# Kernel optimization log

Hardware: AMD Instinct MI355X
Metric: run time of the kernel (lower is better)

The kernel has to match this reference:

```python
import jax, jax.numpy as jnp
import numpy as np

B = 8192
DB, DA, DE, DM, DS = 512, 256, 256, 512, 512
IN = DB + DA + DE + DM + DS  # 2048
F = 2048


def _ternary_linear(x, w, b):
    # BitNet-b1.58 absmean quantization with straight-through estimator.
    s = jnp.mean(jnp.abs(w))
    wq = jnp.round(jnp.clip(w / (s + 1e-5), -1.0, 1.0)) * s
    wq = w + jax.lax.stop_gradient(wq - w)  # STE
    return x @ wq.T + b


def _layernorm(x, g, b, eps=1e-5):
    m = jnp.mean(x, axis=-1, keepdims=True)
    v = jnp.mean((x - m) ** 2, axis=-1, keepdims=True)
    return (x - m) * jax.lax.rsqrt(v + eps) * g + b


def _gelu(x):
    return jax.nn.gelu(x, approximate=False)  # torch nn.GELU default (erf)


def setup_inputs() -> dict:
    key = jax.random.key(0)
    ks = jax.random.split(key, 16)
    w = lambda k, o, i: (jax.random.normal(k, (o, i), dtype=jnp.float32) * 0.02)
    return {
        "z_byte": jax.random.normal(ks[0], (B, DB), dtype=jnp.float32),
        "z_addr": jax.random.normal(ks[1], (B, DA), dtype=jnp.float32),
        "z_evt": jax.random.normal(ks[2], (B, DE), dtype=jnp.float32),
        "z_map": jax.random.normal(ks[3], (B, DM), dtype=jnp.float32),
        "z_sum": jax.random.normal(ks[4], (B, DS), dtype=jnp.float32),
        "gate_w1": w(ks[5], F, IN), "gate_b1": jnp.zeros((F,), jnp.float32),
        "gate_w2": w(ks[6], F, F), "gate_b2": jnp.zeros((F,), jnp.float32),
        "tr_w1": w(ks[7], F, IN), "tr_b1": jnp.zeros((F,), jnp.float32),
        "tr_w2": w(ks[8], F, F), "tr_b2": jnp.zeros((F,), jnp.float32),
        "mlp_w1": w(ks[9], 2 * F, F), "mlp_b1": jnp.zeros((2 * F,), jnp.float32),
        "mlp_w2": w(ks[10], F, 2 * F), "mlp_b2": jnp.zeros((F,), jnp.float32),
        "ln1_g": jnp.ones((F,), jnp.float32), "ln1_b": jnp.zeros((F,), jnp.float32),
        "ln2_g": jnp.ones((F,), jnp.float32), "ln2_b": jnp.zeros((F,), jnp.float32),
    }


def reference(z_byte, z_addr, z_evt, z_map, z_sum,
              gate_w1, gate_b1, gate_w2, gate_b2,
              tr_w1, tr_b1, tr_w2, tr_b2,
              mlp_w1, mlp_b1, mlp_w2, mlp_b2,
              ln1_g, ln1_b, ln2_g, ln2_b):
    combined = jnp.concatenate([z_byte, z_addr, z_evt, z_map, z_sum], axis=-1)  # [B, IN]
    g = _ternary_linear(_gelu(_ternary_linear(combined, gate_w1, gate_b1)), gate_w2, gate_b2)
    t = _ternary_linear(_gelu(_ternary_linear(combined, tr_w1, tr_b1)), tr_w2, tr_b2)
    fused = jax.nn.sigmoid(g * 1.2) * t
    fused = _layernorm(fused, ln1_g, ln1_b)
    mlp = _gelu(fused @ mlp_w1.T + mlp_b1) @ mlp_w2.T + mlp_b2
    return _layernorm(fused + mlp, ln2_g, ln2_b)
```

## Files before the change

### kernel.cpp

```cpp
#include <hip/hip_runtime.h>

typedef unsigned short u16;
typedef unsigned int u32;
typedef __bf16 bf16x8 __attribute__((ext_vector_type(8)));
typedef float f32x4 __attribute__((ext_vector_type(4)));
typedef const __attribute__((address_space(3))) u16* ldsp;

#define B_ROWS 8192

__device__ __forceinline__ float bf2f(u16 h) {
    union { u32 u; float f; } v; v.u = ((u32)h) << 16; return v.f;
}
__device__ __forceinline__ u16 f2bf(float f) {
    union { float f; u32 u; } v; v.f = f;
    u32 r = v.u + 0x7fffu + ((v.u >> 16) & 1u);
    return (u16)(r >> 16);
}
__device__ __forceinline__ float gelu_fast(float x) {
    float u = x * (0.7978845608f + 0.0356774081f * x * x);
    float e = __expf(2.f * u);
    float th = 1.f - 2.f / (e + 1.f);
    return 0.5f * x * (1.f + th);
}
__device__ __forceinline__ float sigmoid12(float g) {
    return 1.f / (1.f + __expf(-1.2f * g));
}
__device__ __forceinline__ float wave_reduce_sum(float v) {
    #pragma unroll
    for (int m = 32; m; m >>= 1) v += __shfl_xor(v, m, 64);
    return v;
}
__device__ __forceinline__ void async16(const void* g, void* l) {
    __builtin_amdgcn_global_load_lds((const __attribute__((address_space(1))) u32*)g,
                                     (__attribute__((address_space(3))) u32*)l, 16, 0, 0);
}
template<int OFF>
__device__ __forceinline__ bf16x8 dsr(ldsp a) {
    bf16x8 r;
    asm volatile("ds_read_b128 %0, %1 offset:%c2"
                 : "=v"(r) : "v"(a), "i"(OFF) : "memory");
    return r;
}

__global__ void absmean1_kernel(const float* __restrict__ w0, const float* __restrict__ w1,
                                const float* __restrict__ w2, const float* __restrict__ w3,
                                float* __restrict__ partials) {
    const float* w = (blockIdx.y == 0) ? w0 : (blockIdx.y == 1) ? w1 : (blockIdx.y == 2) ? w2 : w3;
    int base = blockIdx.x * 16384;
    float acc = 0.f;
    for (int j = threadIdx.x; j < 16384; j += 256) {
        float4 v = ((const float4*)w)[base + j];
        acc += fabsf(v.x) + fabsf(v.y) + fabsf(v.z) + fabsf(v.w);
    }
    acc = wave_reduce_sum(acc);
    __shared__ float red[4];
    int lane = threadIdx.x & 63, wv = threadIdx.x >> 6;
    if (lane == 0) red[wv] = acc;
    __syncthreads();
    if (threadIdx.x == 0)
        partials[blockIdx.y * 64 + blockIdx.x] = red[0] + red[1] + red[2] + red[3];
}

__global__ void absmean2_kernel(const float* __restrict__ partials, double* __restrict__ sums) {
    float v = partials[blockIdx.x * 64 + threadIdx.x];
    v = wave_reduce_sum(v);
    if (threadIdx.x == 0) sums[blockIdx.x] = (double)v;
}

__global__ void prep_kernel(const float* __restrict__ w0, const float* __restrict__ w1,
                            const float* __restrict__ w2, const float* __restrict__ w3,
                            const float* __restrict__ mw1, const float* __restrict__ mw2,
                            u16* __restrict__ wq, u16* __restrict__ mwq,
                            const double* __restrict__ sums) {
    int y = blockIdx.y;
    int i = blockIdx.x * 256 + threadIdx.x;
    if (y < 4) {
        const float* w = (y == 0) ? w0 : (y == 1) ? w1 : (y == 2) ? w2 : w3;
        float s = (float)(sums[y] * (1.0 / 4194304.0));
        float den = s + 1e-5f;
        float4 v = ((const float4*)w)[i];
        ushort4 o;
        o.x = f2bf(rintf(fminf(fmaxf(v.x / den, -1.f), 1.f)));
        o.y = f2bf(rintf(fminf(fmaxf(v.y / den, -1.f), 1.f)));
        o.z = f2bf(rintf(fminf(fmaxf(v.z / den, -1.f), 1.f)));
        o.w = f2bf(rintf(fminf(fmaxf(v.w / den, -1.f), 1.f)));
        ((ushort4*)(wq + (size_t)y * 4194304))[i] = o;
    } else {
        const float* src = (y == 4) ? mw1 : mw2;
        u16* dst = mwq + (y == 4 ? 0 : 8388608);
        #pragma unroll
        for (int r = 0; r < 2; ++r) {
            int j = i + r * 1048576;
            float4 v = ((const float4*)src)[j];
            ushort4 o = {f2bf(v.x), f2bf(v.y), f2bf(v.z), f2bf(v.w)};
            ((ushort4*)dst)[j] = o;
        }
    }
}

__global__ void concat_kernel(const float* __restrict__ zb, const float* __restrict__ za,
                              const float* __restrict__ ze, const float* __restrict__ zm,
                              const float* __restrict__ zs, u16* __restrict__ out) {
    int row = blockIdx.x, t = threadIdx.x;
    int col = t * 8;
    const float* src; int scol, stride;
    if (col < 512)       { src = zb; scol = col;        stride = 512; }
    else if (col < 768)  { src = za; scol = col - 512;  stride = 256; }
    else if (col < 1024) { src = ze; scol = col - 768;  stride = 256; }
    else if (col < 1536) { src = zm; scol = col - 1024; stride = 512; }
    else                 { src = zs; scol = col - 1536; stride = 512; }
    const float4* s4 = (const float4*)(src + (size_t)row * stride + scol);
    float4 a = s4[0], b = s4[1];
    ushort4 p0 = {f2bf(a.x), f2bf(a.y), f2bf(a.z), f2bf(a.w)};
    ushort4 p1 = {f2bf(b.x), f2bf(b.y), f2bf(b.z), f2bf(b.w)};
    u16* o = out + (size_t)row * 2048 + col;
    *(ushort4*)o = p0;
    *(ushort4*)(o + 4) = p1;
}

#define STG_A(d, h, kt_) { \
    async16(Ab0 + (size_t)(h) * ha + (size_t)(kt_) * 64, &lds[0][d][h][ci0 * 8]); \
    async16(Ab1 + (size_t)(h) * ha + (size_t)(kt_) * 64, &lds[0][d][h][ci1 * 8]); }
#define STG_B(d, h, kt_) { \
    async16(Wb0 + (size_t)(h) * hw + (size_t)(kt_) * 64, &lds[1][d][h][ci0 * 8]); \
    async16(Wb1 + (size_t)(h) * hw + (size_t)(kt_) * 64, &lds[1][d][h][ci1 * 8]); }
#define AOFF(d, qm, fm) (((d) * 2 + (qm)) * 16384 + (fm) * 2048)
#define BOFF(d, qn, fn) (((d) * 2 + (qn)) * 16384 + (fn) * 2048)
#define LDA_ALL(d, qm) { \
    af[0][0] = dsr<AOFF(d,qm,0)>(vA0); af[0][1] = dsr<AOFF(d,qm,0)>(vA1); \
    af[1][0] = dsr<AOFF(d,qm,1)>(vA0); af[1][1] = dsr<AOFF(d,qm,1)>(vA1); \
    af[2][0] = dsr<AOFF(d,qm,2)>(vA0); af[2][1] = dsr<AOFF(d,qm,2)>(vA1); \
    af[3][0] = dsr<AOFF(d,qm,3)>(vA0); af[3][1] = dsr<AOFF(d,qm,3)>(vA1); }
#define LDB_H(d, qn) { \
    bf[qn][0][0] = dsr<BOFF(d,qn,0)>(vB0); bf[qn][0][1] = dsr<BOFF(d,qn,0)>(vB1); \
    bf[qn][1][0] = dsr<BOFF(d,qn,1)>(vB0); bf[qn][1][1] = dsr<BOFF(d,qn,1)>(vB1); }
#define MFMA_PH(qm, qn) { \
    _Pragma("unroll") for (int fm = 0; fm < 4; ++fm) \
    _Pragma("unroll") for (int fn = 0; fn < 2; ++fn) { \
        acc[qm][qn][fm][fn] = __builtin_amdgcn_mfma_f32_16x16x32_bf16(af[fm][0], bf[qn][fn][0], acc[qm][qn][fm][fn], 0, 0, 0); \
        acc[qm][qn][fm][fn] = __builtin_amdgcn_mfma_f32_16x16x32_bf16(af[fm][1], bf[qn][fn][1], acc[qm][qn][fm][fn], 0, 0, 0); } }
#define PH_TAIL(qm, qn) \
    __builtin_amdgcn_s_barrier(); \
    asm volatile("s_waitcnt lgkmcnt(0)" ::: "memory"); \
    __builtin_amdgcn_sched_barrier(0); \
    __builtin_amdgcn_s_setprio(1); \
    MFMA_PH(qm, qn); \
    __builtin_amdgcn_s_setprio(0); \
    __builtin_amdgcn_s_barrier();
#define GROUP(ktv, d, e) { \
    LDA_ALL(d, 0); LDB_H(d, 0); \
    if ((ktv) + 1 < NT) { STG_B(e, 0, (ktv) + 1); STG_A(e, 1, (ktv) + 1); } \
    PH_TAIL(0, 0); \
    LDB_H(d, 1); \
    PH_TAIL(0, 1); \
    LDA_ALL(d, 1); \
    if ((ktv) + 2 < NT) STG_A(d, 0, (ktv) + 2); \
    PH_TAIL(1, 1); \
    if ((ktv) + 2 < NT) STG_B(d, 1, (ktv) + 2); \
    __builtin_amdgcn_s_barrier(); \
    __builtin_amdgcn_s_setprio(1); \
    MFMA_PH(1, 0); \
    __builtin_amdgcn_s_setprio(0); \
    if ((ktv) < NT - 2)       { asm volatile("s_waitcnt vmcnt(4)" ::: "memory"); } \
    else if ((ktv) == NT - 2) { asm volatile("s_waitcnt vmcnt(0)" ::: "memory"); } \
    __builtin_amdgcn_s_barrier(); }

template<int EPI>
__global__ __launch_bounds__(512, 2) void gemm256(
        const u16* __restrict__ A, const u16* __restrict__ A2, int lda,
        const u16* __restrict__ W, int wz,
        const float* __restrict__ bias0, const float* __restrict__ bias1,
        void* out, void* out2,
        const double* sum0, const double* sum1,
        int N, int K, int ncut) {
    __shared__ __align__(16) u16 lds[2][2][2][8192];
    if (blockIdx.z) { A = A2; W += wz; out = out2; bias0 = bias1; sum0 = sum1; }

    const int t = threadIdx.x;
    const int l = t & 63;
    const int w = t >> 6;
    const int lr = l & 15, quad = l >> 4;
    const int wm = w >> 2, wn = w & 3;
    const int NT = K >> 6;

    const int nwg  = gridDim.x * gridDim.y;
    const int flat = blockIdx.y * gridDim.x + blockIdx.x;
    const int swz  = (flat & 7) * (nwg >> 3) + (flat >> 3);
    const int bn0 = (swz % gridDim.x) * 256, bm0 = (swz / gridDim.x) * 256;

    const int ci0 = t, ci1 = 512 + t;
    const int row0 = ci0 >> 3, row1 = ci1 >> 3;
    const int cg0 = (ci0 & 7) ^ (row0 & 7);
    const int cg1 = (ci1 & 7) ^ (row1 & 7);
    const u16* Ab0 = A + (size_t)(bm0 + row0) * lda + cg0 * 8;
    const u16* Ab1 = A + (size_t)(bm0 + row1) * lda + cg1 * 8;
    const u16* Wb0 = W + (size_t)(bn0 + row0) * K + cg0 * 8;
    const u16* Wb1 = W + (size_t)(bn0 + row1) * K + cg1 * 8;
    const size_t ha = (size_t)128 * lda;
    const size_t hw = (size_t)128 * K;

    const int r0a = wm * 64 + lr;
    const int cA0u = ((quad) ^ (r0a & 7)) * 8;
    const int r0b = wn * 32 + lr;
    const int cB0u = ((quad) ^ (r0b & 7)) * 8;
    ldsp lb = (ldsp)&lds[0][0][0][0];
    ldsp vA0 = lb + r0a * 64 + cA0u;
    ldsp vA1 = lb + r0a * 64 + (cA0u ^ 32);
    ldsp vB0 = lb + 32768 + r0b * 64 + cB0u;
    ldsp vB1 = lb + 32768 + r0b * 64 + (cB0u ^ 32);

    f32x4 acc[2][2][4][2] = {};
    bf16x8 af[4][2];
    bf16x8 bf[2][2][2];

    STG_A(0, 0, 0); STG_B(0, 0, 0); STG_B(0, 1, 0); STG_A(0, 1, 0);
    asm volatile("" ::: "memory");
    STG_A(1, 0, 1); STG_B(1, 1, 1);
    asm volatile("s_waitcnt vmcnt(4)" ::: "memory");
    __builtin_amdgcn_s_barrier();

    for (int kt = 0; kt < NT; kt += 2) {
        GROUP(kt, 0, 1);
        GROUP(kt + 1, 1, 0);
    }

    float s0 = sum0 ? (float)(*sum0 * (1.0 / 4194304.0)) : 1.f;
    float s1 = sum1 ? (float)(*sum1 * (1.0 / 4194304.0)) : 1.f;
    #pragma unroll
    for (int qn = 0; qn < 2; ++qn) {
        #pragma unroll
        for (int fn = 0; fn < 2; ++fn) {
            int gcol = bn0 + qn * 128 + wn * 32 + fn * 16 + lr;
            bool lo = gcol < ncut;
            float bv = lo ? bias0[gcol] : bias1[gcol - ncut];
            float sc = lo ? s0 : s1;
            #pragma unroll
            for (int qm = 0; qm < 2; ++qm) {
                #pragma unroll
                for (int fm = 0; fm < 4; ++fm) {
                    #pragma unroll
                    for (int i = 0; i < 4; ++i) {
                        int grow = bm0 + qm * 128 + wm * 64 + fm * 16 + quad * 4 + i;
                        size_t idx = (size_t)grow * N + gcol;
                        float v = acc[qm][qn][fm][fn][i] * sc + bv;
                        if (EPI == 0)      ((u16*)out)[idx]   = f2bf(gelu_fast(v));
                        else if (EPI == 1) ((float*)out)[idx] = v;
                        else               ((u16*)out)[idx]   = f2bf(v);
                    }
                }
            }
        }
    }
}

__global__ void ln1_kernel(const u16* __restrict__ g, const u16* tt,
                           u16* outb,
                           const float* __restrict__ gam, const float* __restrict__ bet) {
    int row = blockIdx.x, t = threadIdx.x;
    int c0 = t * 8;
    uint4 gv = *(const uint4*)(g  + (size_t)row * 2048 + c0);
    uint4 tv = *(const uint4*)(tt + (size_t)row * 2048 + c0);
    u32 gw[4] = {gv.x, gv.y, gv.z, gv.w}, tw[4] = {tv.x, tv.y, tv.z, tv.w};
    float f[8];
    #pragma unroll
    for (int j = 0; j < 4; ++j) {
        f[2 * j]     = sigmoid12(bf2f((u16)(gw[j] & 0xffff))) * bf2f((u16)(tw[j] & 0xffff));
        f[2 * j + 1] = sigmoid12(bf2f((u16)(gw[j] >> 16)))    * bf2f((u16)(tw[j] >> 16));
    }
    float s1 = 0.f, s2 = 0.f;
    #pragma unroll
    for (int j = 0; j < 8; ++j) { s1 += f[j]; s2 += f[j] * f[j]; }
    s1 = wave_reduce_sum(s1); s2 = wave_reduce_sum(s2);
    __shared__ float red[8];
    int lane = t & 63, wv = t >> 6;
    if (lane == 0) { red[wv] = s1; red[4 + wv] = s2; }
    __syncthreads();
    float S1 = red[0] + red[1] + red[2] + red[3];
    float S2 = red[4] + red[5] + red[6] + red[7];
    float mean = S1 * (1.f / 2048.f);
    float var = S2 * (1.f / 2048.f) - mean * mean;
    float r = rsqrtf(var + 1e-5f);
    u16 ob[8];
    #pragma unroll
    for (int j = 0; j < 8; ++j)
        ob[j] = f2bf((f[j] - mean) * r * gam[c0 + j] + bet[c0 + j]);
    *(uint4*)(outb + (size_t)row * 2048 + c0) = *(uint4*)ob;
}

__global__ void ln2_kernel(const u16* __restrict__ fb, float* io,
                           const float* __restrict__ gam, const float* __restrict__ bet) {
    int row = blockIdx.x, t = threadIdx.x;
    int c0 = t * 8;
    uint4 fv = *(const uint4*)(fb + (size_t)row * 2048 + c0);
    u32 fw[4] = {fv.x, fv.y, fv.z, fv.w};
    float4* iov = (float4*)(io + (size_t)row * 2048 + c0);
    float4 m0 = iov[0], m1 = iov[1];
    float x[8] = {m0.x, m0.y, m0.z, m0.w, m1.x, m1.y, m1.z, m1.w};
    #pragma unroll
    for (int j = 0; j < 4; ++j) {
        x[2 * j]     += bf2f((u16)(fw[j] & 0xffff));
        x[2 * j + 1] += bf2f((u16)(fw[j] >> 16));
    }
    float s1 = 0.f, s2 = 0.f;
    #pragma unroll
    for (int j = 0; j < 8; ++j) { s1 += x[j]; s2 += x[j] * x[j]; }
    s1 = wave_reduce_sum(s1); s2 = wave_reduce_sum(s2);
    __shared__ float red[8];
    int lane = t & 63, wv = t >> 6;
    if (lane == 0) { red[wv] = s1; red[4 + wv] = s2; }
    __syncthreads();
    float S1 = red[0] + red[1] + red[2] + red[3];
    float S2 = red[4] + red[5] + red[6] + red[7];
    float mean = S1 * (1.f / 2048.f);
    float var = S2 * (1.f / 2048.f) - mean * mean;
    float r = rsqrtf(var + 1e-5f);
    float o[8];
    #pragma unroll
    for (int j = 0; j < 8; ++j)
        o[j] = (x[j] - mean) * r * gam[c0 + j] + bet[c0 + j];
    iov[0] = make_float4(o[0], o[1], o[2], o[3]);
    iov[1] = make_float4(o[4], o[5], o[6], o[7]);
}

extern "C" void kernel_launch(void* const* d_in, const int* in_sizes, int n_in,
                              void* d_out, int out_size, void* d_ws, size_t ws_size,
                              hipStream_t stream) {
    const float* zb  = (const float*)d_in[0];
    const float* za  = (const float*)d_in[1];
    const float* ze  = (const float*)d_in[2];
    const float* zm  = (const float*)d_in[3];
    const float* zs  = (const float*)d_in[4];
    const float* gw1 = (const float*)d_in[5];  const float* gb1 = (const float*)d_in[6];
    const float* gw2 = (const float*)d_in[7];  const float* gb2 = (const float*)d_in[8];
    const float* tw1 = (const float*)d_in[9];  const float* tb1 = (const float*)d_in[10];
    const float* tw2 = (const float*)d_in[11]; const float* tb2 = (const float*)d_in[12];
    const float* mw1 = (const float*)d_in[13]; const float* mb1 = (const float*)d_in[14];
    const float* mw2 = (const float*)d_in[15]; const float* mb2 = (const float*)d_in[16];
    const float* l1g = (const float*)d_in[17]; const float* l1b = (const float*)d_in[18];
    const float* l2g = (const float*)d_in[19]; const float* l2b = (const float*)d_in[20];

    char* wsb = (char*)d_ws;
    u16*   combined = (u16*)(wsb + 0);
    u16*   gbuf     = (u16*)(wsb + 0);
    u16*   wq       = (u16*)(wsb + 33554432);
    u16*   tbuf     = (u16*)(wsb + 67108864);
    u16*   fusedb   = (u16*)(wsb + 67108864);
    u16*   mwq      = (u16*)(wsb + 100663296);
    u16*   HgHt     = (u16*)(wsb + 134217728);
    u16*   M1       = (u16*)(wsb + 134217728);
    float* partials = (float*)(wsb + 134217728);
    double* sums    = (double*)(wsb + 201326592);
    float* mlp2     = (float*)d_out;

    absmean1_kernel<<<dim3(64, 4), 256, 0, stream>>>(gw1, tw1, gw2, tw2, partials);
    absmean2_kernel<<<4, 64, 0, stream>>>(partials, sums);
    prep_kernel<<<dim3(4096, 6), 256, 0, stream>>>(gw1, tw1, gw2, tw2, mw1, mw2, wq, mwq, sums);
    concat_kernel<<<B_ROWS, 256, 0, stream>>>(zb, za, ze, zm, zs, combined);

    gemm256<0><<<dim3(16, 32, 1), 512, 0, stream>>>(
        combined, nullptr, 2048, wq, 0, gb1, tb1, HgHt, nullptr,
        &sums[0], &sums[1], 4096, 2048, 2048);
    gemm256<3><<<dim3(8, 32, 2), 512, 0, stream>>>(
        HgHt, HgHt + 2048, 4096, wq + 8388608, 4194304, gb2, tb2, gbuf, tbuf,
        &sums[2], &sums[3], 2048, 2048, 2048);
    ln1_kernel<<<B_ROWS, 256, 0, stream>>>(gbuf, tbuf, fusedb, l1g, l1b);
    gemm256<0><<<dim3(16, 32, 1), 512, 0, stream>>>(
        fusedb, nullptr, 2048, mwq, 0, mb1, mb1, M1, nullptr,
        nullptr, nullptr, 4096, 2048, 4096);
    gemm256<1><<<dim3(8, 32, 1), 512, 0, stream>>>(
        M1, nullptr, 4096, mwq + 8388608, 0, mb2, mb2, mlp2, nullptr,
        nullptr, nullptr, 2048, 4096, 2048);
    ln2_kernel<<<B_ROWS, 256, 0, stream>>>(fusedb, mlp2, l2g, l2b);
}
```

Baseline: 818.9 us.

## Restructure GEMM main loop to one-barrier-per-tile with fine-grained lgkmcnt waits

Replaces the four-phase per-tile schedule, which had several barriers and partial prefetch two tiles ahead, with a simpler double-buffered loop. All LDS fragment reads for a tile are issued up front, the whole next tile is staged, and MFMAs start under incremental lgkmcnt waits. The loop ends with a full vmcnt(0) wait and a single barrier. This cuts barrier count and overlaps LDS read latency with MFMAs, but prefetch depth drops from two tiles to one, so global load latency may be exposed at the vmcnt(0) wait.

```diff
diff --git a/kernel.cpp b/kernel.cpp
--- a/kernel.cpp
+++ b/kernel.cpp
@@ -124,46 +124,50 @@
 #define STG_B(d, h, kt_) { \
     async16(Wb0 + (size_t)(h) * hw + (size_t)(kt_) * 64, &lds[1][d][h][ci0 * 8]); \
     async16(Wb1 + (size_t)(h) * hw + (size_t)(kt_) * 64, &lds[1][d][h][ci1 * 8]); }
-#define AOFF(d, qm, fm) (((d) * 2 + (qm)) * 16384 + (fm) * 2048)
-#define BOFF(d, qn, fn) (((d) * 2 + (qn)) * 16384 + (fn) * 2048)
-#define LDA_ALL(d, qm) { \
-    af[0][0] = dsr<AOFF(d,qm,0)>(vA0); af[0][1] = dsr<AOFF(d,qm,0)>(vA1); \
-    af[1][0] = dsr<AOFF(d,qm,1)>(vA0); af[1][1] = dsr<AOFF(d,qm,1)>(vA1); \
-    af[2][0] = dsr<AOFF(d,qm,2)>(vA0); af[2][1] = dsr<AOFF(d,qm,2)>(vA1); \
-    af[3][0] = dsr<AOFF(d,qm,3)>(vA0); af[3][1] = dsr<AOFF(d,qm,3)>(vA1); }
+#define AOFF(d, h, fm) (((d) * 2 + (h)) * 16384 + (fm) * 2048)
+#define BOFF(d, h, fn) (((d) * 2 + (h)) * 16384 + (fn) * 2048)
+#define LDA2(d, h, fm) { \
+    af[fm][0] = dsr<AOFF(d,h,fm)>(vA0); af[fm][1] = dsr<AOFF(d,h,fm)>(vA1); }
 #define LDB_H(d, qn) { \
     bf[qn][0][0] = dsr<BOFF(d,qn,0)>(vB0); bf[qn][0][1] = dsr<BOFF(d,qn,0)>(vB1); \
     bf[qn][1][0] = dsr<BOFF(d,qn,1)>(vB0); bf[qn][1][1] = dsr<BOFF(d,qn,1)>(vB1); }
-#define MFMA_PH(qm, qn) { \
-    _Pragma("unroll") for (int fm = 0; fm < 4; ++fm) \
-    _Pragma("unroll") for (int fn = 0; fn < 2; ++fn) { \
-        acc[qm][qn][fm][fn] = __builtin_amdgcn_mfma_f32_16x16x32_bf16(af[fm][0], bf[qn][fn][0], acc[qm][qn][fm][fn], 0, 0, 0); \
-        acc[qm][qn][fm][fn] = __builtin_amdgcn_mfma_f32_16x16x32_bf16(af[fm][1], bf[qn][fn][1], acc[qm][qn][fm][fn], 0, 0, 0); } }
-#define PH_TAIL(qm, qn) \
+#define W_LGKM(n) { \
+    asm volatile("s_waitcnt lgkmcnt(" n ")" ::: "memory"); \
+    __builtin_amdgcn_sched_barrier(0); }
+#define MFMA1(qm, qn, fm, fn, ks) \
+    acc[qm][qn][fm][fn] = __builtin_amdgcn_mfma_f32_16x16x32_bf16(af[fm][ks], bf[qn][fn][ks], acc[qm][qn][fm][fn], 0, 0, 0);
+#define MFMA4(qm, qn, fm) { \
+    MFMA1(qm, qn, fm, 0, 0); MFMA1(qm, qn, fm, 0, 1); \
+    MFMA1(qm, qn, fm, 1, 0); MFMA1(qm, qn, fm, 1, 1); }
+#define MFMA8(qm, qn, fn) { \
+    MFMA1(qm, qn, 0, fn, 0); MFMA1(qm, qn, 0, fn, 1); \
+    MFMA1(qm, qn, 1, fn, 0); MFMA1(qm, qn, 1, fn, 1); \
+    MFMA1(qm, qn, 2, fn, 0); MFMA1(qm, qn, 2, fn, 1); \
+    MFMA1(qm, qn, 3, fn, 0); MFMA1(qm, qn, 3, fn, 1); }
+#define MFMA16(qm, qn) { MFMA4(qm, qn, 0); MFMA4(qm, qn, 1); MFMA4(qm, qn, 2); MFMA4(qm, qn, 3); }
+#define GROUP(ktv, d, e) { \
+    LDA2(d, 0, 0); \
+    LDB_H(d, 0); \
+    LDA2(d, 0, 1); LDA2(d, 0, 2); LDA2(d, 0, 3); \
+    LDB_H(d, 1); \
+    if ((ktv) + 1 < NT) { \
+        STG_A(e, 0, (ktv) + 1); STG_B(e, 0, (ktv) + 1); \
+        STG_B(e, 1, (ktv) + 1); STG_A(e, 1, (ktv) + 1); } \
+    W_LGKM("10"); __builtin_amdgcn_s_setprio(1); MFMA4(0, 0, 0); \
+    W_LGKM("8");  MFMA4(0, 0, 1); \
+    W_LGKM("6");  MFMA4(0, 0, 2); \
+    W_LGKM("4");  MFMA4(0, 0, 3); \
+    W_LGKM("2");  MFMA8(0, 1, 0); \
+    W_LGKM("0");  MFMA8(0, 1, 1); __builtin_amdgcn_s_setprio(0); \
+    LDA2(d, 1, 0); LDA2(d, 1, 1); LDA2(d, 1, 2); LDA2(d, 1, 3); \
+    W_LGKM("6"); __builtin_amdgcn_s_setprio(1); MFMA4(1, 1, 0); \
+    W_LGKM("4"); MFMA4(1, 1, 1); \
+    W_LGKM("2"); MFMA4(1, 1, 2); \
+    W_LGKM("0"); MFMA4(1, 1, 3); \
+    MFMA16(1, 0); __builtin_amdgcn_s_setprio(0); \
+    asm volatile("s_waitcnt vmcnt(0)" ::: "memory"); \
     __builtin_amdgcn_s_barrier(); \
-    asm volatile("s_waitcnt lgkmcnt(0)" ::: "memory"); \
-    __builtin_amdgcn_sched_barrier(0); \
-    __builtin_amdgcn_s_setprio(1); \
-    MFMA_PH(qm, qn); \
-    __builtin_amdgcn_s_setprio(0); \
-    __builtin_amdgcn_s_barrier();
-#define GROUP(ktv, d, e) { \
-    LDA_ALL(d, 0); LDB_H(d, 0); \
-    if ((ktv) + 1 < NT) { STG_B(e, 0, (ktv) + 1); STG_A(e, 1, (ktv) + 1); } \
-    PH_TAIL(0, 0); \
-    LDB_H(d, 1); \
-    PH_TAIL(0, 1); \
-    LDA_ALL(d, 1); \
-    if ((ktv) + 2 < NT) STG_A(d, 0, (ktv) + 2); \
-    PH_TAIL(1, 1); \
-    if ((ktv) + 2 < NT) STG_B(d, 1, (ktv) + 2); \
-    __builtin_amdgcn_s_barrier(); \
-    __builtin_amdgcn_s_setprio(1); \
-    MFMA_PH(1, 0); \
-    __builtin_amdgcn_s_setprio(0); \
-    if ((ktv) < NT - 2)       { asm volatile("s_waitcnt vmcnt(4)" ::: "memory"); } \
-    else if ((ktv) == NT - 2) { asm volatile("s_waitcnt vmcnt(0)" ::: "memory"); } \
-    __builtin_amdgcn_s_barrier(); }
+    __builtin_amdgcn_sched_barrier(0); }
 
 template<int EPI>
 __global__ __launch_bounds__(512, 2) void gemm256(
@@ -214,10 +218,9 @@
     bf16x8 bf[2][2][2];
 
     STG_A(0, 0, 0); STG_B(0, 0, 0); STG_B(0, 1, 0); STG_A(0, 1, 0);
-    asm volatile("" ::: "memory");
-    STG_A(1, 0, 1); STG_B(1, 1, 1);
-    asm volatile("s_waitcnt vmcnt(4)" ::: "memory");
+    asm volatile("s_waitcnt vmcnt(0)" ::: "memory");
     __builtin_amdgcn_s_barrier();
+    __builtin_amdgcn_sched_barrier(0);
 
     for (int kt = 0; kt < NT; kt += 2) {
         GROUP(kt, 0, 1);
```

New measurement: 827.1 us. Within noise of the previous version (+1.0%).
